# Optimization experiments

Measured on AMD Instinct MI355X. Metric: run time of the kernel, lower is better.

Reference implementation:

```python
import jax, jax.numpy as jnp
import numpy as np

N, E, F0, HEADS, B, OUT = 100000, 1600000, 128, 4, 64, 32
CHANNELS = [16, 8, 4, 2]
NEG_SLOPE = 0.2


def setup_inputs() -> dict:
    key = jax.random.key(0)
    ks = jax.random.split(key, 40)
    inp = {}
    inp['x'] = jax.random.normal(ks[0], (N, F0), dtype=jnp.float32)
    inp['edge_index'] = jax.random.randint(ks[1], (2, E), 0, N, dtype=jnp.int64)
    inp['batch'] = jnp.sort(jax.random.randint(ks[2], (N,), 0, B, dtype=jnp.int64))
    # GATConv params per layer: W [in, heads*out], att_src/att_dst [heads, out], bias [heads*out]
    in_dim = F0
    ki = 3
    for li, oc in enumerate(CHANNELS, start=1):
        scale = 1.0 / np.sqrt(in_dim)
        inp[f'W{li}'] = jax.random.normal(ks[ki], (in_dim, HEADS * oc), dtype=jnp.float32) * scale
        inp[f'a_src{li}'] = jax.random.normal(ks[ki + 1], (HEADS, oc), dtype=jnp.float32) * 0.1
        inp[f'a_dst{li}'] = jax.random.normal(ks[ki + 2], (HEADS, oc), dtype=jnp.float32) * 0.1
        inp[f'b{li}'] = jnp.zeros((HEADS * oc,), dtype=jnp.float32)
        ki += 3
        in_dim = HEADS * oc
    inp['W_fc'] = jax.random.normal(ks[ki], (2 * HEADS, OUT), dtype=jnp.float32) * (1.0 / np.sqrt(2 * HEADS))
    inp['b_fc'] = jnp.zeros((OUT,), dtype=jnp.float32)
    return inp


def gat_layer(x, src, dst, W, a_src, a_dst, b, oc):
    n = x.shape[0]
    h = (x @ W).reshape(n, HEADS, oc)                    # [N, H, C]
    al_s = jnp.einsum('nhc,hc->nh', h, a_src)            # [N, H]
    al_d = jnp.einsum('nhc,hc->nh', h, a_dst)
    e = jax.nn.leaky_relu(al_s[src] + al_d[dst], NEG_SLOPE)  # [E, H]
    # segment softmax over incoming edges per destination node
    m = jax.ops.segment_max(e, dst, num_segments=n)
    m = jnp.where(jnp.isfinite(m), m, 0.0)
    ex = jnp.exp(e - m[dst])
    s = jax.ops.segment_sum(ex, dst, num_segments=n)
    alpha = ex / (s[dst] + 1e-16)                        # [E, H]
    out = jax.ops.segment_sum(h[src] * alpha[:, :, None], dst, num_segments=n)
    return out.reshape(n, HEADS * oc) + b


def reference(x, edge_index, batch, W1, a_src1, a_dst1, b1, W2, a_src2, a_dst2, b2,
              W3, a_src3, a_dst3, b3, W4, a_src4, a_dst4, b4, W_fc, b_fc):
    n = x.shape[0]
    loops = jnp.arange(n, dtype=edge_index.dtype)
    src = jnp.concatenate([edge_index[0], loops])   # PyG GATConv adds self-loops
    dst = jnp.concatenate([edge_index[1], loops])
    params = [(W1, a_src1, a_dst1, b1), (W2, a_src2, a_dst2, b2),
              (W3, a_src3, a_dst3, b3), (W4, a_src4, a_dst4, b4)]
    h = x
    for (W, a_s, a_d, b), oc in zip(params, CHANNELS):
        h = jax.nn.relu(gat_layer(h, src, dst, W, a_s, a_d, b, oc))
        # dropout(0.3) is identity at inference
    # global mean pool over graphs in the batch
    sums = jax.ops.segment_sum(h, batch, num_segments=B)
    cnt = jax.ops.segment_sum(jnp.ones((n,), h.dtype), batch, num_segments=B)
    pooled = sums / jnp.maximum(cnt, 1.0)[:, None]
    return pooled @ W_fc + b_fc
```

## Files before the change

kernel.cpp:

```cpp
#include <hip/hip_runtime.h>
#include <hip/hip_bf16.h>

#define NNODES 100000
#define NEDGES 1600000
#define NHEADS 4
#define NGRAPH 64
#define NOUTF  32
#define BSH    9
#define NBUK   ((NNODES + 511) >> 9)
#define BPAD   16
#define BCAP   9216
#define CGRID  512
#define G1GRID ((NNODES + 63) / 64)

__device__ __forceinline__ unsigned short f2bf(float f) {
    union { float f; unsigned u; } v;
    v.f = f;
    unsigned r = v.u + 0x7FFF + ((v.u >> 16) & 1);
    return (unsigned short)(r >> 16);
}
__device__ __forceinline__ float bflo(unsigned u) {
    union { unsigned u; float f; } v;
    v.u = u << 16;
    return v.f;
}
__device__ __forceinline__ float bfhi(unsigned u) {
    union { unsigned u; float f; } v;
    v.u = u & 0xFFFF0000u;
    return v.f;
}

__device__ __forceinline__ bool ei_is_int64(const int* __restrict__ ei) {
    int acc = 0;
    #pragma unroll
    for (int i = 0; i < 32; i++) acc |= ei[2 * i + 1];
    return acc == 0;
}

__device__ __forceinline__ void fma4(float4& a, float s, const float4& b) {
    a.x += s * b.x;
    a.y += s * b.y;
    a.z += s * b.z;
    a.w += s * b.w;
}

__global__ __launch_bounds__(256) void gat_coarse_gemm1_kernel(
        const int* __restrict__ ei, const int* __restrict__ bt,
        int* __restrict__ bkcur, int* __restrict__ packed, int* __restrict__ bat,
        const float* __restrict__ x, const float* __restrict__ W1,
        const float* __restrict__ as1, const float* __restrict__ ad1,
        unsigned short* __restrict__ h1, float* __restrict__ al_s,
        float* __restrict__ al_d, int ne, int n) {
    __shared__ float smem[64 * 64 + 64 * 132];
    const int tid = threadIdx.x;
    if (blockIdx.x < CGRID) {
        int* hist = (int*)smem;
        int* base = hist + NBUK;
        for (int i = tid; i < NBUK; i += 256) hist[i] = 0;
        __syncthreads();
        bool wide = ei_is_int64(ei);
        int chunk = (ne + CGRID - 1) / CGRID;
        int e0 = blockIdx.x * chunk;
        int e1 = min(e0 + chunk, ne);
        for (int i = e0 + tid; i < e1; i += 256) {
            int d = wide ? ei[2 * (ne + i)] : ei[ne + i];
            atomicAdd(&hist[d >> BSH], 1);
        }
        __syncthreads();
        for (int i = tid; i < NBUK; i += 256)
            base[i] = hist[i] ? atomicAdd(&bkcur[i * BPAD], hist[i]) : 0;
        __syncthreads();
        for (int i = tid; i < NBUK; i += 256) hist[i] = 0;
        __syncthreads();
        for (int i = e0 + tid; i < e1; i += 256) {
            int s = wide ? ei[2 * i] : ei[i];
            int d = wide ? ei[2 * (ne + i)] : ei[ne + i];
            int bk = d >> BSH;
            int pos = base[bk] + atomicAdd(&hist[bk], 1);
            if (pos < BCAP) packed[bk * BCAP + pos] = s | ((d & 511) << 17);
        }
        int gid = blockIdx.x * 256 + tid;
        for (int i = gid; i < n; i += CGRID * 256) bat[i] = wide ? bt[2 * i] : bt[i];
    } else {
        constexpr int DIN = 128, DOUT = 64, KTILE = 64;
        constexpr int OG = DOUT / 4;
        constexpr int NPB = 64;
        constexpr int S = DIN + 4;
        constexpr int C = DOUT / NHEADS;
        float* Wl = smem;
        float* xs = smem + KTILE * DOUT;
        const int base = (blockIdx.x - CGRID) * NPB;
        constexpr int KC = DIN / 4;
        for (int i = tid; i < NPB * KC; i += 256) {
            int nn = i / KC, kc = i - nn * KC;
            int nd = base + nn;
            float4 v = (nd < n) ? ((const float4*)x)[(size_t)nd * KC + kc]
                                : make_float4(0.f, 0.f, 0.f, 0.f);
            *(float4*)&xs[nn * S + kc * 4] = v;
        }
        const int og = tid % OG;
        const int ng = tid / OG;
        const int n0 = ng * 4;
        float4 acc[4] = {};
        for (int kt = 0; kt < DIN; kt += KTILE) {
            __syncthreads();
            for (int i = tid; i < KTILE * OG; i += 256)
                ((float4*)Wl)[i] = ((const float4*)W1)[kt * OG + i];
            __syncthreads();
            #pragma unroll 2
            for (int k = 0; k < KTILE; k += 4) {
                float4 wv[4], xv[4];
                #pragma unroll
                for (int j = 0; j < 4; j++)
                    wv[j] = *(const float4*)&Wl[(k + j) * DOUT + og * 4];
                #pragma unroll
                for (int r = 0; r < 4; r++)
                    xv[r] = *(const float4*)&xs[(n0 + r) * S + kt + k];
                #pragma unroll
                for (int r = 0; r < 4; r++) {
                    fma4(acc[r], xv[r].x, wv[0]);
                    fma4(acc[r], xv[r].y, wv[1]);
                    fma4(acc[r], xv[r].z, wv[2]);
                    fma4(acc[r], xv[r].w, wv[3]);
                }
            }
        }
        float4 asv = ((const float4*)as1)[og];
        float4 adv = ((const float4*)ad1)[og];
        #pragma unroll
        for (int r = 0; r < 4; r++) {
            int node = base + n0 + r;
            bool ok = node < n;
            if (ok) {
                ushort4 o;
                o.x = f2bf(acc[r].x);
                o.y = f2bf(acc[r].y);
                o.z = f2bf(acc[r].z);
                o.w = f2bf(acc[r].w);
                ((ushort4*)h1)[(size_t)node * OG + og] = o;
            }
            float ps = acc[r].x * asv.x + acc[r].y * asv.y + acc[r].z * asv.z + acc[r].w * asv.w;
            float pd = acc[r].x * adv.x + acc[r].y * adv.y + acc[r].z * adv.z + acc[r].w * adv.w;
            #pragma unroll
            for (int off = 1; off < C / 4; off <<= 1) {
                ps += __shfl_xor(ps, off);
                pd += __shfl_xor(pd, off);
            }
            if (ok && (og % (C / 4)) == 0) {
                int hh = og / (C / 4);
                al_s[node * NHEADS + hh] = ps;
                al_d[node * NHEADS + hh] = pd;
            }
        }
    }
}

__global__ __launch_bounds__(1024) void gat_fine_kernel(
        const int* __restrict__ packed, const int* __restrict__ bkcur,
        int* __restrict__ row_ptr, int* __restrict__ col, int n) {
    __shared__ int bscan[256];
    __shared__ int dg[512];
    __shared__ int excl[512];
    __shared__ int partial[256];
    __shared__ int cur[512];
    int b = blockIdx.x;
    int tid = threadIdx.x;
    if (tid < 256) bscan[tid] = (tid < NBUK) ? bkcur[tid * BPAD] : 0;
    if (tid < 512) dg[tid] = 0;
    __syncthreads();
    for (int off = 1; off < 256; off <<= 1) {
        int u = (tid < 256 && tid >= off) ? bscan[tid - off] : 0;
        __syncthreads();
        if (tid < 256) bscan[tid] += u;
        __syncthreads();
    }
    int cntb = bkcur[b * BPAD];
    int csr0 = bscan[b] - cntb;
    int pbeg = b * BCAP;
    int pend = pbeg + cntb;
    for (int t = pbeg + tid; t < pend; t += 1024)
        atomicAdd(&dg[packed[t] >> 17], 1);
    __syncthreads();
    int a0 = 0, a1 = 0, s = 0;
    if (tid < 256) {
        a0 = dg[2 * tid];
        a1 = dg[2 * tid + 1];
        s = a0 + a1;
        partial[tid] = s;
    }
    __syncthreads();
    for (int off = 1; off < 256; off <<= 1) {
        int u = (tid < 256 && tid >= off) ? partial[tid - off] : 0;
        __syncthreads();
        if (tid < 256) partial[tid] += u;
        __syncthreads();
    }
    if (tid < 256) {
        int ebase = partial[tid] - s;
        excl[2 * tid] = ebase;
        excl[2 * tid + 1] = ebase + a0;
        cur[2 * tid] = ebase;
        cur[2 * tid + 1] = ebase + a0;
    }
    __syncthreads();
    int node0 = b << BSH;
    if (tid < 512) {
        int nd = node0 + tid;
        if (nd < n) row_ptr[nd] = csr0 + excl[tid];
    }
    if (b == NBUK - 1 && tid == 0) row_ptr[n] = bscan[NBUK - 1];
    for (int t = pbeg + tid; t < pend; t += 1024) {
        int v = packed[t];
        int pos = atomicAdd(&cur[v >> 17], 1);
        col[csr0 + pos] = v & 0x1FFFF;
    }
}

template<int DIN, int DOUT, int KTILE, bool BF16OUT>
__global__ __launch_bounds__(256) void gat_gemm_attn_kernel(
        const float* __restrict__ in, const float* __restrict__ W,
        const float* __restrict__ a_src, const float* __restrict__ a_dst,
        void* __restrict__ hout, float* __restrict__ al_s, float* __restrict__ al_d, int n) {
    constexpr int OG = DOUT / 4;
    constexpr int NPB = 1024 / OG;
    constexpr int S = DIN + 4;
    constexpr int C = DOUT / NHEADS;
    __shared__ float Wl[KTILE * DOUT];
    __shared__ float xs[NPB * S];
    const int tid = threadIdx.x;
    const int base = blockIdx.x * NPB;
    constexpr int KC = DIN / 4;
    for (int i = tid; i < NPB * KC; i += 256) {
        int nn = i / KC, kc = i - nn * KC;
        int nd = base + nn;
        float4 v = (nd < n) ? ((const float4*)in)[(size_t)nd * KC + kc]
                            : make_float4(0.f, 0.f, 0.f, 0.f);
        *(float4*)&xs[nn * S + kc * 4] = v;
    }
    const int og = tid % OG;
    const int ng = tid / OG;
    const int n0 = ng * 4;
    float4 acc[4] = {};
    for (int kt = 0; kt < DIN; kt += KTILE) {
        __syncthreads();
        for (int i = tid; i < KTILE * OG; i += 256)
            ((float4*)Wl)[i] = ((const float4*)W)[kt * OG + i];
        __syncthreads();
        #pragma unroll 2
        for (int k = 0; k < KTILE; k += 4) {
            float4 wv[4], xv[4];
            #pragma unroll
            for (int j = 0; j < 4; j++)
                wv[j] = *(const float4*)&Wl[(k + j) * DOUT + og * 4];
            #pragma unroll
            for (int r = 0; r < 4; r++)
                xv[r] = *(const float4*)&xs[(n0 + r) * S + kt + k];
            #pragma unroll
            for (int r = 0; r < 4; r++) {
                fma4(acc[r], xv[r].x, wv[0]);
                fma4(acc[r], xv[r].y, wv[1]);
                fma4(acc[r], xv[r].z, wv[2]);
                fma4(acc[r], xv[r].w, wv[3]);
            }
        }
    }
    float4 asv = ((const float4*)a_src)[og];
    float4 adv = ((const float4*)a_dst)[og];
    #pragma unroll
    for (int r = 0; r < 4; r++) {
        int node = base + n0 + r;
        bool ok = node < n;
        if (ok) {
            if constexpr (BF16OUT) {
                ushort4 o;
                o.x = f2bf(acc[r].x);
                o.y = f2bf(acc[r].y);
                o.z = f2bf(acc[r].z);
                o.w = f2bf(acc[r].w);
                ((ushort4*)hout)[(size_t)node * OG + og] = o;
            } else {
                ((float4*)hout)[(size_t)node * OG + og] = acc[r];
            }
        }
        if constexpr (C >= 4) {
            float ps = acc[r].x * asv.x + acc[r].y * asv.y + acc[r].z * asv.z + acc[r].w * asv.w;
            float pd = acc[r].x * adv.x + acc[r].y * adv.y + acc[r].z * adv.z + acc[r].w * adv.w;
            #pragma unroll
            for (int off = 1; off < C / 4; off <<= 1) {
                ps += __shfl_xor(ps, off);
                pd += __shfl_xor(pd, off);
            }
            if (ok && (og % (C / 4)) == 0) {
                int hh = og / (C / 4);
                al_s[node * NHEADS + hh] = ps;
                al_d[node * NHEADS + hh] = pd;
            }
        } else {
            if (ok) {
                al_s[node * NHEADS + 2 * og]     = acc[r].x * asv.x + acc[r].y * asv.y;
                al_s[node * NHEADS + 2 * og + 1] = acc[r].z * asv.z + acc[r].w * asv.w;
                al_d[node * NHEADS + 2 * og]     = acc[r].x * adv.x + acc[r].y * adv.y;
                al_d[node * NHEADS + 2 * og + 1] = acc[r].z * adv.z + acc[r].w * adv.w;
            }
        }
    }
}

template<int C>
__global__ __launch_bounds__(256) void gat_agg_bf16_kernel(
        const unsigned short* __restrict__ h, const float* __restrict__ al_s,
        const float* __restrict__ al_d, const int* __restrict__ row_ptr,
        const int* __restrict__ col, const float* __restrict__ bias,
        float* __restrict__ out, int n) {
    constexpr int G = NHEADS * C;
    constexpr int L = G / 8;
    constexpr int NG = 64 / L;
    int lane = threadIdx.x & 63;
    int nodeA = blockIdx.x * 8 + (threadIdx.x >> 6) * 2;
    if (nodeA >= n) return;
    bool hasB = (nodeA + 1) < n;
    int nodeB = hasB ? nodeA + 1 : nodeA;
    int sub = lane & (L - 1);
    int g = lane / L;
    int hh = (sub * 8) / C;
    int begA = row_ptr[nodeA];
    int cntA = row_ptr[nodeA + 1] - begA;
    int begB = row_ptr[nodeB];
    int cntB = row_ptr[nodeB + 1] - begB;
    float aldA = al_d[nodeA * NHEADS + hh];
    float aldB = al_d[nodeB * NHEADS + hh];
    const uint4* h4 = (const uint4*)h;
    float aA[8] = {}, aB[8] = {};
    float wsA = 0.f, wsB = 0.f;
    int tend = max(cntA, cntB) + 1;
    for (int t = g; t < tend; t += NG) {
        int srcA = (t < cntA) ? col[begA + t] : nodeA;
        int srcB = (t < cntB) ? col[begB + t] : nodeB;
        float eA = al_s[srcA * NHEADS + hh] + aldA;
        float eB = al_s[srcB * NHEADS + hh] + aldB;
        uint4 hvA = h4[(size_t)srcA * L + sub];
        uint4 hvB = h4[(size_t)srcB * L + sub];
        eA = (eA > 0.f) ? eA : 0.2f * eA;
        eB = (eB > 0.f) ? eB : 0.2f * eB;
        float wA = (t <= cntA) ? __expf(eA) : 0.f;
        float wB = (hasB && t <= cntB) ? __expf(eB) : 0.f;
        wsA += wA;
        aA[0] += wA * bflo(hvA.x);
        aA[1] += wA * bfhi(hvA.x);
        aA[2] += wA * bflo(hvA.y);
        aA[3] += wA * bfhi(hvA.y);
        aA[4] += wA * bflo(hvA.z);
        aA[5] += wA * bfhi(hvA.z);
        aA[6] += wA * bflo(hvA.w);
        aA[7] += wA * bfhi(hvA.w);
        wsB += wB;
        aB[0] += wB * bflo(hvB.x);
        aB[1] += wB * bfhi(hvB.x);
        aB[2] += wB * bflo(hvB.y);
        aB[3] += wB * bfhi(hvB.y);
        aB[4] += wB * bflo(hvB.z);
        aB[5] += wB * bfhi(hvB.z);
        aB[6] += wB * bflo(hvB.w);
        aB[7] += wB * bfhi(hvB.w);
    }
    #pragma unroll
    for (int off = L; off < 64; off <<= 1) {
        #pragma unroll
        for (int k = 0; k < 8; k++) {
            aA[k] += __shfl_xor(aA[k], off);
            aB[k] += __shfl_xor(aB[k], off);
        }
        wsA += __shfl_xor(wsA, off);
        wsB += __shfl_xor(wsB, off);
    }
    if (g == 0) {
        int j0 = sub * 8;
        float4 bv0 = *(const float4*)&bias[j0];
        float4 bv1 = *(const float4*)&bias[j0 + 4];
        {
            float inv = 1.f / (wsA + 1e-16f);
            float4 o0, o1;
            o0.x = aA[0] * inv + bv0.x;
            o0.y = aA[1] * inv + bv0.y;
            o0.z = aA[2] * inv + bv0.z;
            o0.w = aA[3] * inv + bv0.w;
            o1.x = aA[4] * inv + bv1.x;
            o1.y = aA[5] * inv + bv1.y;
            o1.z = aA[6] * inv + bv1.z;
            o1.w = aA[7] * inv + bv1.w;
            o0.x = (o0.x > 0.f) ? o0.x : 0.f;
            o0.y = (o0.y > 0.f) ? o0.y : 0.f;
            o0.z = (o0.z > 0.f) ? o0.z : 0.f;
            o0.w = (o0.w > 0.f) ? o0.w : 0.f;
            o1.x = (o1.x > 0.f) ? o1.x : 0.f;
            o1.y = (o1.y > 0.f) ? o1.y : 0.f;
            o1.z = (o1.z > 0.f) ? o1.z : 0.f;
            o1.w = (o1.w > 0.f) ? o1.w : 0.f;
            *(float4*)&out[(size_t)nodeA * G + j0] = o0;
            *(float4*)&out[(size_t)nodeA * G + j0 + 4] = o1;
        }
        if (hasB) {
            float inv = 1.f / (wsB + 1e-16f);
            float4 o0, o1;
            o0.x = aB[0] * inv + bv0.x;
            o0.y = aB[1] * inv + bv0.y;
            o0.z = aB[2] * inv + bv0.z;
            o0.w = aB[3] * inv + bv0.w;
            o1.x = aB[4] * inv + bv1.x;
            o1.y = aB[5] * inv + bv1.y;
            o1.z = aB[6] * inv + bv1.z;
            o1.w = aB[7] * inv + bv1.w;
            o0.x = (o0.x > 0.f) ? o0.x : 0.f;
            o0.y = (o0.y > 0.f) ? o0.y : 0.f;
            o0.z = (o0.z > 0.f) ? o0.z : 0.f;
            o0.w = (o0.w > 0.f) ? o0.w : 0.f;
            o1.x = (o1.x > 0.f) ? o1.x : 0.f;
            o1.y = (o1.y > 0.f) ? o1.y : 0.f;
            o1.z = (o1.z > 0.f) ? o1.z : 0.f;
            o1.w = (o1.w > 0.f) ? o1.w : 0.f;
            *(float4*)&out[(size_t)nodeB * G + j0] = o0;
            *(float4*)&out[(size_t)nodeB * G + j0 + 4] = o1;
        }
    }
}

__global__ __launch_bounds__(256) void gat_agg_bf16_c4_kernel(
        const unsigned short* __restrict__ h, const float* __restrict__ al_s,
        const float* __restrict__ al_d, const int* __restrict__ row_ptr,
        const int* __restrict__ col, const float* __restrict__ bias,
        float* __restrict__ out, int n) {
    constexpr int G = 16;
    constexpr int L = 4;
    constexpr int NG = 16;
    int lane = threadIdx.x & 63;
    int nodeA = blockIdx.x * 8 + (threadIdx.x >> 6) * 2;
    if (nodeA >= n) return;
    bool hasB = (nodeA + 1) < n;
    int nodeB = hasB ? nodeA + 1 : nodeA;
    int sub = lane & (L - 1);
    int g = lane / L;
    int begA = row_ptr[nodeA];
    int cntA = row_ptr[nodeA + 1] - begA;
    int begB = row_ptr[nodeB];
    int cntB = row_ptr[nodeB + 1] - begB;
    float aldA = al_d[nodeA * NHEADS + sub];
    float aldB = al_d[nodeB * NHEADS + sub];
    const uint2* h2 = (const uint2*)h;
    float aA[4] = {}, aB[4] = {};
    float wsA = 0.f, wsB = 0.f;
    int tend = max(cntA, cntB) + 1;
    for (int t = g; t < tend; t += NG) {
        int srcA = (t < cntA) ? col[begA + t] : nodeA;
        int srcB = (t < cntB) ? col[begB + t] : nodeB;
        float eA = al_s[srcA * NHEADS + sub] + aldA;
        float eB = al_s[srcB * NHEADS + sub] + aldB;
        uint2 hvA = h2[(size_t)srcA * L + sub];
        uint2 hvB = h2[(size_t)srcB * L + sub];
        eA = (eA > 0.f) ? eA : 0.2f * eA;
        eB = (eB > 0.f) ? eB : 0.2f * eB;
        float wA = (t <= cntA) ? __expf(eA) : 0.f;
        float wB = (hasB && t <= cntB) ? __expf(eB) : 0.f;
        wsA += wA;
        aA[0] += wA * bflo(hvA.x);
        aA[1] += wA * bfhi(hvA.x);
        aA[2] += wA * bflo(hvA.y);
        aA[3] += wA * bfhi(hvA.y);
        wsB += wB;
        aB[0] += wB * bflo(hvB.x);
        aB[1] += wB * bfhi(hvB.x);
        aB[2] += wB * bflo(hvB.y);
        aB[3] += wB * bfhi(hvB.y);
    }
    #pragma unroll
    for (int off = L; off < 64; off <<= 1) {
        #pragma unroll
        for (int k = 0; k < 4; k++) {
            aA[k] += __shfl_xor(aA[k], off);
            aB[k] += __shfl_xor(aB[k], off);
        }
        wsA += __shfl_xor(wsA, off);
        wsB += __shfl_xor(wsB, off);
    }
    if (g == 0) {
        int j0 = sub * 4;
        float4 bv = *(const float4*)&bias[j0];
        {
            float inv = 1.f / (wsA + 1e-16f);
            float4 o;
            o.x = aA[0] * inv + bv.x;
            o.y = aA[1] * inv + bv.y;
            o.z = aA[2] * inv + bv.z;
            o.w = aA[3] * inv + bv.w;
            o.x = (o.x > 0.f) ? o.x : 0.f;
            o.y = (o.y > 0.f) ? o.y : 0.f;
            o.z = (o.z > 0.f) ? o.z : 0.f;
            o.w = (o.w > 0.f) ? o.w : 0.f;
            *(float4*)&out[(size_t)nodeA * G + j0] = o;
        }
        if (hasB) {
            float inv = 1.f / (wsB + 1e-16f);
            float4 o;
            o.x = aB[0] * inv + bv.x;
            o.y = aB[1] * inv + bv.y;
            o.z = aB[2] * inv + bv.z;
            o.w = aB[3] * inv + bv.w;
            o.x = (o.x > 0.f) ? o.x : 0.f;
            o.y = (o.y > 0.f) ? o.y : 0.f;
            o.z = (o.z > 0.f) ? o.z : 0.f;
            o.w = (o.w > 0.f) ? o.w : 0.f;
            *(float4*)&out[(size_t)nodeB * G + j0] = o;
        }
    }
}

template<int C>
__global__ __launch_bounds__(256) void gat_agg_kernel(
        const float* __restrict__ h, const float* __restrict__ al_s, const float* __restrict__ al_d,
        const int* __restrict__ row_ptr, const int* __restrict__ col,
        const float* __restrict__ bias, float* __restrict__ out, int n) {
    constexpr int G = NHEADS * C;
    constexpr int L = G / 4;
    constexpr int NG = 64 / L;
    int lane = threadIdx.x & 63;
    int nodeA = blockIdx.x * 8 + (threadIdx.x >> 6) * 2;
    if (nodeA >= n) return;
    bool hasB = (nodeA + 1) < n;
    int nodeB = hasB ? nodeA + 1 : nodeA;
    int sub = lane & (L - 1);
    int g = lane / L;
    int c0 = sub * 4;
    int begA = row_ptr[nodeA];
    int cntA = row_ptr[nodeA + 1] - begA;
    int begB = row_ptr[nodeB];
    int cntB = row_ptr[nodeB + 1] - begB;
    float ald0A = al_d[nodeA * NHEADS + c0 / C];
    float ald1A = al_d[nodeA * NHEADS + (c0 + 2) / C];
    float ald0B = al_d[nodeB * NHEADS + c0 / C];
    float ald1B = al_d[nodeB * NHEADS + (c0 + 2) / C];
    const float4* h4 = (const float4*)h;
    float4 accA = make_float4(0.f, 0.f, 0.f, 0.f);
    float4 accB = make_float4(0.f, 0.f, 0.f, 0.f);
    float ws0A = 0.f, ws1A = 0.f, ws0B = 0.f, ws1B = 0.f;
    int tend = max(cntA, cntB) + 1;
    for (int t = g; t < tend; t += NG) {
        int srcA = (t < cntA) ? col[begA + t] : nodeA;
        int srcB = (t < cntB) ? col[begB + t] : nodeB;
        float4 hvA = h4[srcA * L + sub];
        float4 hvB = h4[srcB * L + sub];
        float e0A = al_s[srcA * NHEADS + c0 / C] + ald0A;
        float e1A = al_s[srcA * NHEADS + (c0 + 2) / C] + ald1A;
        float e0B = al_s[srcB * NHEADS + c0 / C] + ald0B;
        float e1B = al_s[srcB * NHEADS + (c0 + 2) / C] + ald1B;
        e0A = (e0A > 0.f) ? e0A : 0.2f * e0A;
        e1A = (e1A > 0.f) ? e1A : 0.2f * e1A;
        e0B = (e0B > 0.f) ? e0B : 0.2f * e0B;
        e1B = (e1B > 0.f) ? e1B : 0.2f * e1B;
        bool okA = (t <= cntA);
        bool okB = (hasB && t <= cntB);
        float w0A = okA ? __expf(e0A) : 0.f;
        float w1A = okA ? __expf(e1A) : 0.f;
        float w0B = okB ? __expf(e0B) : 0.f;
        float w1B = okB ? __expf(e1B) : 0.f;
        ws0A += w0A;
        ws1A += w1A;
        accA.x += w0A * hvA.x;
        accA.y += w0A * hvA.y;
        accA.z += w1A * hvA.z;
        accA.w += w1A * hvA.w;
        ws0B += w0B;
        ws1B += w1B;
        accB.x += w0B * hvB.x;
        accB.y += w0B * hvB.y;
        accB.z += w1B * hvB.z;
        accB.w += w1B * hvB.w;
    }
    #pragma unroll
    for (int off = L; off < 64; off <<= 1) {
        accA.x += __shfl_xor(accA.x, off);
        accA.y += __shfl_xor(accA.y, off);
        accA.z += __shfl_xor(accA.z, off);
        accA.w += __shfl_xor(accA.w, off);
        accB.x += __shfl_xor(accB.x, off);
        accB.y += __shfl_xor(accB.y, off);
        accB.z += __shfl_xor(accB.z, off);
        accB.w += __shfl_xor(accB.w, off);
        ws0A += __shfl_xor(ws0A, off);
        ws1A += __shfl_xor(ws1A, off);
        ws0B += __shfl_xor(ws0B, off);
        ws1B += __shfl_xor(ws1B, off);
    }
    if (g == 0) {
        float4 bv = ((const float4*)bias)[sub];
        {
            float4 v;
            v.x = accA.x / (ws0A + 1e-16f) + bv.x;
            v.y = accA.y / (ws0A + 1e-16f) + bv.y;
            v.z = accA.z / (ws1A + 1e-16f) + bv.z;
            v.w = accA.w / (ws1A + 1e-16f) + bv.w;
            v.x = (v.x > 0.f) ? v.x : 0.f;
            v.y = (v.y > 0.f) ? v.y : 0.f;
            v.z = (v.z > 0.f) ? v.z : 0.f;
            v.w = (v.w > 0.f) ? v.w : 0.f;
            ((float4*)out)[nodeA * L + sub] = v;
        }
        if (hasB) {
            float4 v;
            v.x = accB.x / (ws0B + 1e-16f) + bv.x;
            v.y = accB.y / (ws0B + 1e-16f) + bv.y;
            v.z = accB.z / (ws1B + 1e-16f) + bv.z;
            v.w = accB.w / (ws1B + 1e-16f) + bv.w;
            v.x = (v.x > 0.f) ? v.x : 0.f;
            v.y = (v.y > 0.f) ? v.y : 0.f;
            v.z = (v.z > 0.f) ? v.z : 0.f;
            v.w = (v.w > 0.f) ? v.w : 0.f;
            ((float4*)out)[nodeB * L + sub] = v;
        }
    }
}

__global__ __launch_bounds__(256) void gat_poolfc_kernel(
        const float* __restrict__ x, const int* __restrict__ bat,
        const float* __restrict__ Wfc, const float* __restrict__ bfc,
        float* __restrict__ out, int n) {
    __shared__ float sh[256][9];
    int b = blockIdx.x;
    int tid = threadIdx.x;
    int lo = 0, hi = n;
    while (lo < hi) { int mid = (lo + hi) >> 1; if (bat[mid] < b) lo = mid + 1; else hi = mid; }
    int i0 = lo;
    hi = n;
    while (lo < hi) { int mid = (lo + hi) >> 1; if (bat[mid] < b + 1) lo = mid + 1; else hi = mid; }
    int i1 = lo;
    float a[8] = {};
    for (int i = i0 + tid; i < i1; i += 256) {
        float4 v0 = ((const float4*)x)[(size_t)i * 2];
        float4 v1 = ((const float4*)x)[(size_t)i * 2 + 1];
        a[0] += v0.x; a[1] += v0.y; a[2] += v0.z; a[3] += v0.w;
        a[4] += v1.x; a[5] += v1.y; a[6] += v1.z; a[7] += v1.w;
    }
    #pragma unroll
    for (int k = 0; k < 8; k++) sh[tid][k] = a[k];
    __syncthreads();
    for (int off = 128; off >= 1; off >>= 1) {
        if (tid < off)
            #pragma unroll
            for (int k = 0; k < 8; k++) sh[tid][k] += sh[tid + off][k];
        __syncthreads();
    }
    if (tid < NOUTF) {
        float c = (float)(i1 - i0);
        if (c < 1.f) c = 1.f;
        float acc = bfc[tid];
        #pragma unroll
        for (int d = 0; d < 8; d++) acc += (sh[0][d] / c) * Wfc[d * NOUTF + tid];
        out[b * NOUTF + tid] = acc;
    }
}

extern "C" void kernel_launch(void* const* d_in, const int* in_sizes, int n_in,
                              void* d_out, int out_size, void* d_ws, size_t ws_size,
                              hipStream_t stream) {
    const float* x = (const float*)d_in[0];
    const int* ei = (const int*)d_in[1];
    const int* batch = (const int*)d_in[2];
    const float* W1 = (const float*)d_in[3];
    const float* as1 = (const float*)d_in[4];
    const float* ad1 = (const float*)d_in[5];
    const float* b1 = (const float*)d_in[6];
    const float* W2 = (const float*)d_in[7];
    const float* as2 = (const float*)d_in[8];
    const float* ad2 = (const float*)d_in[9];
    const float* b2 = (const float*)d_in[10];
    const float* W3 = (const float*)d_in[11];
    const float* as3 = (const float*)d_in[12];
    const float* ad3 = (const float*)d_in[13];
    const float* b3 = (const float*)d_in[14];
    const float* W4 = (const float*)d_in[15];
    const float* as4 = (const float*)d_in[16];
    const float* ad4 = (const float*)d_in[17];
    const float* b4 = (const float*)d_in[18];
    const float* Wfc = (const float*)d_in[19];
    const float* bfc = (const float*)d_in[20];

    const int n = NNODES, ne = NEDGES;

    char* p = (char*)d_ws;
    auto carve = [&](size_t bytes) {
        char* r = p;
        p += (bytes + 255) & ~(size_t)255;
        return r;
    };
    int* row_ptr = (int*)carve((size_t)(n + 1) * 4);
    int* col = (int*)carve((size_t)ne * 4);
    int* bkcur = (int*)carve(256 * BPAD * 4);
    int* packed = (int*)carve((size_t)NBUK * BCAP * 4);
    float* buf_h = (float*)carve((size_t)n * 64 * 4);
    float* buf_x = (float*)carve((size_t)n * 64 * 4);
    float* al_s = (float*)carve((size_t)n * NHEADS * 4);
    float* al_d = (float*)carve((size_t)n * NHEADS * 4);
    int* bat = (int*)carve((size_t)n * 4);
    unsigned short* h_bf16 = (unsigned short*)buf_h;

    hipMemsetAsync(bkcur, 0, 256 * BPAD * 4, stream);

    gat_coarse_gemm1_kernel<<<CGRID + G1GRID, 256, 0, stream>>>(
        ei, batch, bkcur, packed, bat, x, W1, as1, ad1, h_bf16, al_s, al_d, ne, n);

    gat_fine_kernel<<<NBUK, 1024, 0, stream>>>(packed, bkcur, row_ptr, col, n);

    gat_agg_bf16_kernel<16><<<(n + 7) / 8, 256, 0, stream>>>(
        h_bf16, al_s, al_d, row_ptr, col, b1, buf_x, n);

    gat_gemm_attn_kernel<64, 32, 64, true><<<(n + 127) / 128, 256, 0, stream>>>(
        buf_x, W2, as2, ad2, h_bf16, al_s, al_d, n);
    gat_agg_bf16_kernel<8><<<(n + 7) / 8, 256, 0, stream>>>(
        h_bf16, al_s, al_d, row_ptr, col, b2, buf_x, n);

    gat_gemm_attn_kernel<32, 16, 32, true><<<(n + 255) / 256, 256, 0, stream>>>(
        buf_x, W3, as3, ad3, h_bf16, al_s, al_d, n);
    gat_agg_bf16_c4_kernel<<<(n + 7) / 8, 256, 0, stream>>>(
        h_bf16, al_s, al_d, row_ptr, col, b3, buf_x, n);

    gat_gemm_attn_kernel<16, 8, 16, false><<<(n + 511) / 512, 256, 0, stream>>>(
        buf_x, W4, as4, ad4, buf_h, al_s, al_d, n);
    gat_agg_kernel<2><<<(n + 7) / 8, 256, 0, stream>>>(buf_h, al_s, al_d, row_ptr, col, b4, buf_x, n);

    gat_poolfc_kernel<<<NGRAPH, 256, 0, stream>>>(buf_x, bat, Wfc, bfc, (float*)d_out, n);
}
```

Measured before the change: 384.0 us.

## Store features and attention logits head-major and aggregate one head per launch

Switches layers one and two to a head-major layout for bf16 features and for the source/destination attention logits. Aggregation then runs as a separate launch per head, so each pass gathers from a smaller per-head feature slice with better cache locality. The cost is reading the CSR edge lists and indices once per head, plus more kernel launches. The layer three and four kernels are adjusted to read the head-major logits.

```diff
diff --git a/kernel.cpp b/kernel.cpp
--- a/kernel.cpp
+++ b/kernel.cpp
@@ -127,6 +127,7 @@
         }
         float4 asv = ((const float4*)as1)[og];
         float4 adv = ((const float4*)ad1)[og];
+        constexpr int CH4 = C / 4;
         #pragma unroll
         for (int r = 0; r < 4; r++) {
             int node = base + n0 + r;
@@ -137,19 +138,19 @@
                 o.y = f2bf(acc[r].y);
                 o.z = f2bf(acc[r].z);
                 o.w = f2bf(acc[r].w);
-                ((ushort4*)h1)[(size_t)node * OG + og] = o;
+                ((ushort4*)h1)[(size_t)(og / CH4) * n * CH4 + (size_t)node * CH4 + (og % CH4)] = o;
             }
             float ps = acc[r].x * asv.x + acc[r].y * asv.y + acc[r].z * asv.z + acc[r].w * asv.w;
             float pd = acc[r].x * adv.x + acc[r].y * adv.y + acc[r].z * adv.z + acc[r].w * adv.w;
             #pragma unroll
-            for (int off = 1; off < C / 4; off <<= 1) {
+            for (int off = 1; off < CH4; off <<= 1) {
                 ps += __shfl_xor(ps, off);
                 pd += __shfl_xor(pd, off);
             }
-            if (ok && (og % (C / 4)) == 0) {
-                int hh = og / (C / 4);
-                al_s[node * NHEADS + hh] = ps;
-                al_d[node * NHEADS + hh] = pd;
+            if (ok && (og % CH4) == 0) {
+                int hh = og / CH4;
+                al_s[(size_t)hh * n + node] = ps;
+                al_d[(size_t)hh * n + node] = pd;
             }
         }
     }
@@ -216,7 +217,7 @@
     }
 }
 
-template<int DIN, int DOUT, int KTILE, bool BF16OUT>
+template<int DIN, int DOUT, int KTILE, bool BF16OUT, bool HEADMAJOR>
 __global__ __launch_bounds__(256) void gat_gemm_attn_kernel(
         const float* __restrict__ in, const float* __restrict__ W,
         const float* __restrict__ a_src, const float* __restrict__ a_dst,
@@ -277,7 +278,12 @@
                 o.y = f2bf(acc[r].y);
                 o.z = f2bf(acc[r].z);
                 o.w = f2bf(acc[r].w);
-                ((ushort4*)hout)[(size_t)node * OG + og] = o;
+                if constexpr (HEADMAJOR) {
+                    constexpr int CH4 = C / 4;
+                    ((ushort4*)hout)[(size_t)(og / CH4) * n * CH4 + (size_t)node * CH4 + (og % CH4)] = o;
+                } else {
+                    ((ushort4*)hout)[(size_t)node * OG + og] = o;
+                }
             } else {
                 ((float4*)hout)[(size_t)node * OG + og] = acc[r];
             }
@@ -292,28 +298,31 @@
             }
             if (ok && (og % (C / 4)) == 0) {
                 int hh = og / (C / 4);
-                al_s[node * NHEADS + hh] = ps;
-                al_d[node * NHEADS + hh] = pd;
+                al_s[(size_t)hh * n + node] = ps;
+                al_d[(size_t)hh * n + node] = pd;
             }
         } else {
             if (ok) {
-                al_s[node * NHEADS + 2 * og]     = acc[r].x * asv.x + acc[r].y * asv.y;
-                al_s[node * NHEADS + 2 * og + 1] = acc[r].z * asv.z + acc[r].w * asv.w;
-                al_d[node * NHEADS + 2 * og]     = acc[r].x * adv.x + acc[r].y * adv.y;
-                al_d[node * NHEADS + 2 * og + 1] = acc[r].z * adv.z + acc[r].w * adv.w;
+                al_s[(size_t)(2 * og) * n + node]     = acc[r].x * asv.x + acc[r].y * asv.y;
+                al_s[(size_t)(2 * og + 1) * n + node] = acc[r].z * asv.z + acc[r].w * asv.w;
+                al_d[(size_t)(2 * og) * n + node]     = acc[r].x * adv.x + acc[r].y * adv.y;
+                al_d[(size_t)(2 * og + 1) * n + node] = acc[r].z * adv.z + acc[r].w * adv.w;
             }
         }
     }
 }
 
 template<int C>
-__global__ __launch_bounds__(256) void gat_agg_bf16_kernel(
-        const unsigned short* __restrict__ h, const float* __restrict__ al_s,
-        const float* __restrict__ al_d, const int* __restrict__ row_ptr,
-        const int* __restrict__ col, const float* __restrict__ bias,
-        float* __restrict__ out, int n) {
+__global__ __launch_bounds__(256) void gat_agg_head_kernel(
+        const uint4* __restrict__ hh4,
+        const float* __restrict__ als,
+        const float* __restrict__ ald,
+        const int* __restrict__ row_ptr, const int* __restrict__ col,
+        const float* __restrict__ bias,
+        float* __restrict__ out,
+        int n) {
     constexpr int G = NHEADS * C;
-    constexpr int L = G / 8;
+    constexpr int L = C / 8;
     constexpr int NG = 64 / L;
     int lane = threadIdx.x & 63;
     int nodeA = blockIdx.x * 8 + (threadIdx.x >> 6) * 2;
@@ -322,24 +331,22 @@
     int nodeB = hasB ? nodeA + 1 : nodeA;
     int sub = lane & (L - 1);
     int g = lane / L;
-    int hh = (sub * 8) / C;
     int begA = row_ptr[nodeA];
     int cntA = row_ptr[nodeA + 1] - begA;
     int begB = row_ptr[nodeB];
     int cntB = row_ptr[nodeB + 1] - begB;
-    float aldA = al_d[nodeA * NHEADS + hh];
-    float aldB = al_d[nodeB * NHEADS + hh];
-    const uint4* h4 = (const uint4*)h;
+    float aldA = ald[nodeA];
+    float aldB = ald[nodeB];
     float aA[8] = {}, aB[8] = {};
     float wsA = 0.f, wsB = 0.f;
     int tend = max(cntA, cntB) + 1;
     for (int t = g; t < tend; t += NG) {
         int srcA = (t < cntA) ? col[begA + t] : nodeA;
         int srcB = (t < cntB) ? col[begB + t] : nodeB;
-        float eA = al_s[srcA * NHEADS + hh] + aldA;
-        float eB = al_s[srcB * NHEADS + hh] + aldB;
-        uint4 hvA = h4[(size_t)srcA * L + sub];
-        uint4 hvB = h4[(size_t)srcB * L + sub];
+        float eA = als[srcA] + aldA;
+        float eB = als[srcB] + aldB;
+        uint4 hvA = hh4[(size_t)srcA * L + sub];
+        uint4 hvB = hh4[(size_t)srcB * L + sub];
         eA = (eA > 0.f) ? eA : 0.2f * eA;
         eB = (eB > 0.f) ? eB : 0.2f * eB;
         float wA = (t <= cntA) ? __expf(eA) : 0.f;
@@ -443,8 +450,9 @@
     int cntA = row_ptr[nodeA + 1] - begA;
     int begB = row_ptr[nodeB];
     int cntB = row_ptr[nodeB + 1] - begB;
-    float aldA = al_d[nodeA * NHEADS + sub];
-    float aldB = al_d[nodeB * NHEADS + sub];
+    const float* alsh = al_s + (size_t)sub * n;
+    float aldA = al_d[(size_t)sub * n + nodeA];
+    float aldB = al_d[(size_t)sub * n + nodeB];
     const uint2* h2 = (const uint2*)h;
     float aA[4] = {}, aB[4] = {};
     float wsA = 0.f, wsB = 0.f;
@@ -452,8 +460,8 @@
     for (int t = g; t < tend; t += NG) {
         int srcA = (t < cntA) ? col[begA + t] : nodeA;
         int srcB = (t < cntB) ? col[begB + t] : nodeB;
-        float eA = al_s[srcA * NHEADS + sub] + aldA;
-        float eB = al_s[srcB * NHEADS + sub] + aldB;
+        float eA = alsh[srcA] + aldA;
+        float eB = alsh[srcB] + aldB;
         uint2 hvA = h2[(size_t)srcA * L + sub];
         uint2 hvB = h2[(size_t)srcB * L + sub];
         eA = (eA > 0.f) ? eA : 0.2f * eA;
@@ -528,15 +536,17 @@
     int nodeB = hasB ? nodeA + 1 : nodeA;
     int sub = lane & (L - 1);
     int g = lane / L;
-    int c0 = sub * 4;
+    int h0 = 2 * sub;
     int begA = row_ptr[nodeA];
     int cntA = row_ptr[nodeA + 1] - begA;
     int begB = row_ptr[nodeB];
     int cntB = row_ptr[nodeB + 1] - begB;
-    float ald0A = al_d[nodeA * NHEADS + c0 / C];
-    float ald1A = al_d[nodeA * NHEADS + (c0 + 2) / C];
-    float ald0B = al_d[nodeB * NHEADS + c0 / C];
-    float ald1B = al_d[nodeB * NHEADS + (c0 + 2) / C];
+    const float* als0 = al_s + (size_t)h0 * n;
+    const float* als1 = al_s + (size_t)(h0 + 1) * n;
+    float ald0A = al_d[(size_t)h0 * n + nodeA];
+    float ald1A = al_d[(size_t)(h0 + 1) * n + nodeA];
+    float ald0B = al_d[(size_t)h0 * n + nodeB];
+    float ald1B = al_d[(size_t)(h0 + 1) * n + nodeB];
     const float4* h4 = (const float4*)h;
     float4 accA = make_float4(0.f, 0.f, 0.f, 0.f);
     float4 accB = make_float4(0.f, 0.f, 0.f, 0.f);
@@ -547,10 +557,10 @@
         int srcB = (t < cntB) ? col[begB + t] : nodeB;
         float4 hvA = h4[srcA * L + sub];
         float4 hvB = h4[srcB * L + sub];
-        float e0A = al_s[srcA * NHEADS + c0 / C] + ald0A;
-        float e1A = al_s[srcA * NHEADS + (c0 + 2) / C] + ald1A;
-        float e0B = al_s[srcB * NHEADS + c0 / C] + ald0B;
-        float e1B = al_s[srcB * NHEADS + (c0 + 2) / C] + ald1B;
+        float e0A = als0[srcA] + ald0A;
+        float e1A = als1[srcA] + ald1A;
+        float e0B = als0[srcB] + ald0B;
+        float e1B = als1[srcB] + ald1B;
         e0A = (e0A > 0.f) ? e0A : 0.2f * e0A;
         e1A = (e1A > 0.f) ? e1A : 0.2f * e1A;
         e0B = (e0B > 0.f) ? e0B : 0.2f * e0B;
@@ -708,20 +718,24 @@
 
     gat_fine_kernel<<<NBUK, 1024, 0, stream>>>(packed, bkcur, row_ptr, col, n);
 
-    gat_agg_bf16_kernel<16><<<(n + 7) / 8, 256, 0, stream>>>(
-        h_bf16, al_s, al_d, row_ptr, col, b1, buf_x, n);
-
-    gat_gemm_attn_kernel<64, 32, 64, true><<<(n + 127) / 128, 256, 0, stream>>>(
+    for (int hh = 0; hh < NHEADS; hh++)
+        gat_agg_head_kernel<16><<<(n + 7) / 8, 256, 0, stream>>>(
+            (const uint4*)h_bf16 + (size_t)hh * n * 2, al_s + (size_t)hh * n,
+            al_d + (size_t)hh * n, row_ptr, col, b1 + hh * 16, buf_x + hh * 16, n);
+
+    gat_gemm_attn_kernel<64, 32, 64, true, true><<<(n + 127) / 128, 256, 0, stream>>>(
         buf_x, W2, as2, ad2, h_bf16, al_s, al_d, n);
-    gat_agg_bf16_kernel<8><<<(n + 7) / 8, 256, 0, stream>>>(
-        h_bf16, al_s, al_d, row_ptr, col, b2, buf_x, n);
-
-    gat_gemm_attn_kernel<32, 16, 32, true><<<(n + 255) / 256, 256, 0, stream>>>(
+    for (int hh = 0; hh < NHEADS; hh++)
+        gat_agg_head_kernel<8><<<(n + 7) / 8, 256, 0, stream>>>(
+            (const uint4*)h_bf16 + (size_t)hh * n, al_s + (size_t)hh * n,
+            al_d + (size_t)hh * n, row_ptr, col, b2 + hh * 8, buf_x + hh * 8, n);
+
+    gat_gemm_attn_kernel<32, 16, 32, true, false><<<(n + 255) / 256, 256, 0, stream>>>(
         buf_x, W3, as3, ad3, h_bf16, al_s, al_d, n);
     gat_agg_bf16_c4_kernel<<<(n + 7) / 8, 256, 0, stream>>>(
         h_bf16, al_s, al_d, row_ptr, col, b3, buf_x, n);
 
-    gat_gemm_attn_kernel<16, 8, 16, false><<<(n + 511) / 512, 256, 0, stream>>>(
+    gat_gemm_attn_kernel<16, 8, 16, false, false><<<(n + 511) / 512, 256, 0, stream>>>(
         buf_x, W4, as4, ad4, buf_h, al_s, al_d, n);
     gat_agg_kernel<2><<<(n + 7) / 8, 256, 0, stream>>>(buf_h, al_s, al_d, row_ptr, col, b4, buf_x, n);
 
```

Result: slower. 752.6 us (+96.0%).
